# Kernel optimization log

Hardware: AMD Instinct MI355X
Metric: run time of the kernel (lower is better)

## Reference

```python
import jax, jax.numpy as jnp
import numpy as np

TWO_PI = 6.283185307179586


def setup_inputs() -> dict:
    key = jax.random.key(0)
    k1, k2, k3, k4, k5, k6 = jax.random.split(key, 6)
    B, T, D = 2, 8192, 1024
    x = jax.random.normal(k1, (B, T, D), dtype=jnp.float32)
    # nn.Linear weights are [out, in]; init with small scale like torch default
    s = 1.0 / np.sqrt(D)
    Wk = jax.random.uniform(k2, (D, D), jnp.float32, -s, s)
    Wv = jax.random.uniform(k3, (D, D), jnp.float32, -s, s)
    Wo = jax.random.uniform(k4, (D, D), jnp.float32, -s, s)
    # random phasor frequencies in [0, 2*pi)
    freqs = jax.random.uniform(k5, (D,), jnp.float32, 0.0, TWO_PI)
    return {"x": x, "Wk": Wk, "Wv": Wv, "Wo": Wo, "freqs": freqs}


def reference(x, Wk, Wv, Wo, freqs):
    B, T, C = x.shape
    # k projection is computed in the original forward but never used downstream
    k_real = x @ Wk.T  # [B,T,D] (dead value, kept for fidelity)
    v_real = x @ Wv.T  # [B,T,D]
    v = v_real.astype(jnp.complex64)
    # rotors: per-position unit phasors exp(i * t * freqs), shape [T, D]
    t = jnp.arange(T, dtype=jnp.float32)
    rotors = jnp.exp(1j * (t[:, None] * freqs[None, :])).astype(jnp.complex64)
    # bind each value with its rotor and accumulate causally (O(N) memory trace)
    memory_trace = jnp.cumsum(v * rotors[None, :, :], axis=1)  # [B,T,D] complex64
    # retrieve by unbinding with the conjugate rotor; take the real component
    retrieved = jnp.real(memory_trace * jnp.conj(rotors)[None, :, :])  # [B,T,D]
    return retrieved @ Wo.T
```

## Files before the change

### kernel.cpp

```cpp
#include <hip/hip_runtime.h>
#include <hip/hip_bf16.h>


#define B_  2
#define T_  8192
#define D_  1024
#define BT_ 16384
#define CS_ 32
#define NCHUNK_ 256

typedef __attribute__((ext_vector_type(4))) float f32x4;
typedef __attribute__((ext_vector_type(8))) short bf16x8;

static __device__ inline unsigned short f2bf(float f) {
    union { float f; unsigned int u; } a;
    a.f = f;
    unsigned int u = a.u;
    return (unsigned short)((u + 0x7FFFu + ((u >> 16) & 1u)) >> 16);
}
static __device__ inline float bf2f(unsigned short h) {
    union { unsigned int u; float f; } a;
    a.u = ((unsigned int)h) << 16;
    return a.f;
}

__global__ __launch_bounds__(256) void cast_all(const float* __restrict__ x,
                                                const float* __restrict__ Wv,
                                                const float* __restrict__ Wo,
                                                unsigned short* __restrict__ xb,
                                                unsigned short* __restrict__ wvb,
                                                unsigned short* __restrict__ wob) {
    const int nx = BT_ * D_ / 4;
    const int nw = D_ * D_ / 4;
    int i = blockIdx.x * 256 + threadIdx.x;
    const float4* src;
    unsigned short* dst;
    int j;
    if (i < nx)            { src = (const float4*)x;  dst = xb;  j = i; }
    else if (i < nx + nw)  { src = (const float4*)Wv; dst = wvb; j = i - nx; }
    else                   { src = (const float4*)Wo; dst = wob; j = i - nx - nw; }
    float4 v = src[j];
    ushort4 o;
    o.x = f2bf(v.x); o.y = f2bf(v.y); o.z = f2bf(v.z); o.w = f2bf(v.w);
    ((ushort4*)dst)[j] = o;
}

template <bool BF16OUT>
__global__ __launch_bounds__(256) void gemm_bt(const short* __restrict__ A,
                                               const short* __restrict__ Bm,
                                               void* __restrict__ Cout,
                                               int M, int N, int K) {
    __shared__ short lds[16384];
    const int lane = threadIdx.x & 63;
    const int wave = threadIdx.x >> 6;
    const int wr = wave >> 1, wc = wave & 1;

    const int nb = N >> 7;
    const int id = blockIdx.x;
    const int xcd = id & 7;
    const int slot = id >> 3;
    const int bn = (slot % nb) * 128;
    const int bm = (xcd * ((M >> 7) >> 3) + slot / nb) * 128;

    const int sr = lane >> 3;
    const int cb = lane & 7;
    const short* ga[4];
    const short* gb[4];
#pragma unroll
    for (int cc = 0; cc < 4; ++cc) {
        const int chunk = wave * 4 + cc;
        const int row = chunk * 8 + sr;
        const int col = (cb ^ (row & 7)) * 8;
        ga[cc] = A + (size_t)(bm + row) * K + col;
        gb[cc] = Bm + (size_t)(bn + row) * K + col;
    }

    const int c4r = lane >> 4;
    int aoff[4][2], boff[4][2];
#pragma unroll
    for (int i = 0; i < 4; ++i) {
        const int m = wr * 64 + (lane & 15) + i * 16;
        const int n = wc * 64 + (lane & 15) + i * 16;
#pragma unroll
        for (int ks = 0; ks < 2; ++ks) {
            aoff[i][ks] = m * 64 + (((ks * 4 + c4r) ^ (m & 7)) * 8);
            boff[i][ks] = 8192 + n * 64 + (((ks * 4 + c4r) ^ (n & 7)) * 8);
        }
    }

    f32x4 acc[4][4] = {};

    for (int k0 = 0; k0 < K; k0 += 64) {
#pragma unroll
        for (int cc = 0; cc < 4; ++cc) {
            const int chunk = wave * 4 + cc;
            __builtin_amdgcn_global_load_lds(
                (const __attribute__((address_space(1))) void*)(ga[cc] + k0),
                (__attribute__((address_space(3))) void*)&lds[chunk * 512], 16, 0, 0);
            __builtin_amdgcn_global_load_lds(
                (const __attribute__((address_space(1))) void*)(gb[cc] + k0),
                (__attribute__((address_space(3))) void*)&lds[8192 + chunk * 512], 16, 0, 0);
        }
        __syncthreads();
#pragma unroll
        for (int ks = 0; ks < 2; ++ks) {
            bf16x8 a[4], b[4];
#pragma unroll
            for (int i = 0; i < 4; ++i) a[i] = *(const bf16x8*)&lds[aoff[i][ks]];
#pragma unroll
            for (int j = 0; j < 4; ++j) b[j] = *(const bf16x8*)&lds[boff[j][ks]];
#pragma unroll
            for (int i = 0; i < 4; ++i)
#pragma unroll
                for (int j = 0; j < 4; ++j)
                    acc[i][j] = __builtin_amdgcn_mfma_f32_16x16x32_bf16(a[i], b[j], acc[i][j], 0, 0, 0);
        }
        __syncthreads();
    }

    const int row0 = (lane >> 4) * 4;
#pragma unroll
    for (int i = 0; i < 4; ++i) {
#pragma unroll
        for (int j = 0; j < 4; ++j) {
            const int col = bn + wc * 64 + j * 16 + (lane & 15);
#pragma unroll
            for (int r = 0; r < 4; ++r) {
                const size_t row = bm + wr * 64 + i * 16 + row0 + r;
                if constexpr (BF16OUT)
                    ((unsigned short*)Cout)[row * N + col] = f2bf(acc[i][j][r]);
                else
                    ((float*)Cout)[row * N + col] = acc[i][j][r];
            }
        }
    }
}

__global__ __launch_bounds__(256) void scan_pass1(const unsigned short* __restrict__ v,
                                                  const float* __restrict__ freqs,
                                                  float* __restrict__ csum) {
    const int d0 = threadIdx.x * 4;
    const int chunk = blockIdx.x;
    const int b = blockIdx.y;

    float fr[4], s[4], c[4], sf[4], cf[4], ar[4] = {}, ai[4] = {};
    {
        float4 f4 = *(const float4*)(freqs + d0);
        fr[0] = f4.x; fr[1] = f4.y; fr[2] = f4.z; fr[3] = f4.w;
    }
    const float t0f = (float)(chunk * CS_);
#pragma unroll
    for (int k = 0; k < 4; ++k) {
        sincosf(t0f * fr[k], &s[k], &c[k]);
        sincosf(fr[k], &sf[k], &cf[k]);
    }
    const uint2* vp = (const uint2*)(v + ((size_t)b * T_ + chunk * CS_) * D_ + d0);
    for (int tb = 0; tb < CS_; tb += 8) {
        uint2 w[8];
#pragma unroll
        for (int u = 0; u < 8; ++u) w[u] = vp[(size_t)(tb + u) * (D_ / 4)];
#pragma unroll
        for (int u = 0; u < 8; ++u) {
            float wv[4];
            wv[0] = bf2f((unsigned short)w[u].x);
            wv[1] = bf2f((unsigned short)(w[u].x >> 16));
            wv[2] = bf2f((unsigned short)w[u].y);
            wv[3] = bf2f((unsigned short)(w[u].y >> 16));
#pragma unroll
            for (int k = 0; k < 4; ++k) {
                ar[k] = fmaf(wv[k], c[k], ar[k]);
                ai[k] = fmaf(wv[k], s[k], ai[k]);
                float nc = c[k] * cf[k] - s[k] * sf[k];
                float ns = s[k] * cf[k] + c[k] * sf[k];
                c[k] = nc; s[k] = ns;
            }
        }
    }
    float4* cp = (float4*)(csum + (((size_t)b * NCHUNK_ + chunk) * D_ + d0) * 2);
    float4 o0, o1;
    o0.x = ar[0]; o0.y = ai[0]; o0.z = ar[1]; o0.w = ai[1];
    o1.x = ar[2]; o1.y = ai[2]; o1.z = ar[3]; o1.w = ai[3];
    cp[0] = o0; cp[1] = o1;
}

__global__ __launch_bounds__(256) void scan_pass2(float* __restrict__ csum) {
    const int g = blockIdx.x * 256 + threadIdx.x;
    const int b = g / D_;
    const int d = g % D_;
    float2* cs = (float2*)csum;
    const size_t base = (size_t)b * NCHUNK_ * D_ + d;
    float pr = 0.f, pi = 0.f;
    for (int cc = 0; cc < NCHUNK_; cc += 32) {
        float2 buf[32];
#pragma unroll
        for (int k = 0; k < 32; ++k) buf[k] = cs[base + (size_t)(cc + k) * D_];
#pragma unroll
        for (int k = 0; k < 32; ++k) {
            float r = buf[k].x, im = buf[k].y;
            buf[k] = make_float2(pr, pi);
            pr += r; pi += im;
        }
#pragma unroll
        for (int k = 0; k < 32; ++k) cs[base + (size_t)(cc + k) * D_] = buf[k];
    }
}

__global__ __launch_bounds__(256) void scan_pass3(const unsigned short* __restrict__ v,
                                                  const float* __restrict__ freqs,
                                                  const float* __restrict__ csum,
                                                  unsigned short* __restrict__ ret) {
    const int d0 = threadIdx.x * 4;
    const int chunk = blockIdx.x;
    const int b = blockIdx.y;

    float fr[4], s[4], c[4], sf[4], cf[4], ar[4], ai[4];
    {
        float4 f4 = *(const float4*)(freqs + d0);
        fr[0] = f4.x; fr[1] = f4.y; fr[2] = f4.z; fr[3] = f4.w;
    }
    const float t0f = (float)(chunk * CS_);
#pragma unroll
    for (int k = 0; k < 4; ++k) {
        sincosf(t0f * fr[k], &s[k], &c[k]);
        sincosf(fr[k], &sf[k], &cf[k]);
    }
    {
        const float4* cp = (const float4*)(csum + (((size_t)b * NCHUNK_ + chunk) * D_ + d0) * 2);
        float4 o0 = cp[0], o1 = cp[1];
        ar[0] = o0.x; ai[0] = o0.y; ar[1] = o0.z; ai[1] = o0.w;
        ar[2] = o1.x; ai[2] = o1.y; ar[3] = o1.z; ai[3] = o1.w;
    }
    const uint2* vp = (const uint2*)(v + ((size_t)b * T_ + chunk * CS_) * D_ + d0);
    uint2* rp = (uint2*)(ret + ((size_t)b * T_ + chunk * CS_) * D_ + d0);
    for (int tb = 0; tb < CS_; tb += 8) {
        uint2 w[8];
#pragma unroll
        for (int u = 0; u < 8; ++u) w[u] = vp[(size_t)(tb + u) * (D_ / 4)];
#pragma unroll
        for (int u = 0; u < 8; ++u) {
            float wv[4], o[4];
            wv[0] = bf2f((unsigned short)w[u].x);
            wv[1] = bf2f((unsigned short)(w[u].x >> 16));
            wv[2] = bf2f((unsigned short)w[u].y);
            wv[3] = bf2f((unsigned short)(w[u].y >> 16));
#pragma unroll
            for (int k = 0; k < 4; ++k) {
                ar[k] = fmaf(wv[k], c[k], ar[k]);
                ai[k] = fmaf(wv[k], s[k], ai[k]);
                o[k] = ar[k] * c[k] + ai[k] * s[k];
                float nc = c[k] * cf[k] - s[k] * sf[k];
                float ns = s[k] * cf[k] + c[k] * sf[k];
                c[k] = nc; s[k] = ns;
            }
            uint2 o2;
            o2.x = (unsigned int)f2bf(o[0]) | ((unsigned int)f2bf(o[1]) << 16);
            o2.y = (unsigned int)f2bf(o[2]) | ((unsigned int)f2bf(o[3]) << 16);
            rp[(size_t)(tb + u) * (D_ / 4)] = o2;
        }
    }
}

extern "C" void kernel_launch(void* const* d_in, const int* in_sizes, int n_in,
                              void* d_out, int out_size, void* d_ws, size_t ws_size,
                              hipStream_t stream) {
    const float* x     = (const float*)d_in[0];
    const float* Wv    = (const float*)d_in[2];
    const float* Wo    = (const float*)d_in[3];
    const float* freqs = (const float*)d_in[4];
    float* out = (float*)d_out;

    char* ws = (char*)d_ws;
    unsigned short* x_bf  = (unsigned short*)ws;
    unsigned short* Wv_bf = (unsigned short*)(ws + 33554432);
    unsigned short* Wo_bf = (unsigned short*)(ws + 35651584);
    unsigned short* ret   = (unsigned short*)(ws + 37748736);
    float*          csum  = (float*)(ws + 71303168);
    unsigned short* v_bf = (unsigned short*)d_out;

    cast_all<<<(BT_ * D_ / 4 + 2 * D_ * D_ / 4) / 256, 256, 0, stream>>>(
        x, Wv, Wo, x_bf, Wv_bf, Wo_bf);

    gemm_bt<true><<<(BT_ / 128) * (D_ / 128), 256, 0, stream>>>(
        (const short*)x_bf, (const short*)Wv_bf, (void*)v_bf, BT_, D_, D_);

    dim3 sgrid(NCHUNK_, B_);
    scan_pass1<<<sgrid, 256, 0, stream>>>(v_bf, freqs, csum);
    scan_pass2<<<(B_ * D_) / 256, 256, 0, stream>>>(csum);
    scan_pass3<<<sgrid, 256, 0, stream>>>(v_bf, freqs, csum, ret);

    gemm_bt<false><<<(BT_ / 128) * (D_ / 128), 256, 0, stream>>>(
        (const short*)ret, (const short*)Wo_bf, (void*)out, BT_, D_, D_);
}
```

Baseline: 257.3 us.

## Fuse per-chunk phasor sums into the V-projection GEMM epilogue

The scan's first pass, which computes rotated partial sums per chunk, moves into the epilogue of the V-projection GEMM. Each wave reduces its 64-row tile in registers with rotor recurrences and cross-lane shuffles, then writes the chunk sum directly. This removes one full re-read of the bf16 V tensor and one kernel launch. The chunk size doubles to match the GEMM tile height, and pass 3 is regridded to split D across blocks so its parallelism is unchanged. In exchange, the GEMM epilogue gains sincos and recurrence work, and the longer chunks carry rotor recurrences further, which may cost some accuracy.

```diff
diff --git a/kernel.cpp b/kernel.cpp
--- a/kernel.cpp
+++ b/kernel.cpp
@@ -6,8 +6,8 @@
 #define T_  8192
 #define D_  1024
 #define BT_ 16384
-#define CS_ 32
-#define NCHUNK_ 256
+#define CS_ 64
+#define NCHUNK_ 128
 
 typedef __attribute__((ext_vector_type(4))) float f32x4;
 typedef __attribute__((ext_vector_type(8))) short bf16x8;
@@ -45,10 +45,12 @@
     ((ushort4*)dst)[j] = o;
 }
 
-template <bool BF16OUT>
+template <bool BF16OUT, bool FUSE_SUMS>
 __global__ __launch_bounds__(256) void gemm_bt(const short* __restrict__ A,
                                                const short* __restrict__ Bm,
                                                void* __restrict__ Cout,
+                                               const float* __restrict__ freqs,
+                                               float* __restrict__ csum,
                                                int M, int N, int K) {
     __shared__ short lds[16384];
     const int lane = threadIdx.x & 63;
@@ -118,7 +120,7 @@
         __syncthreads();
     }
 
-    const int row0 = (lane >> 4) * 4;
+    const int row0 = c4r * 4;
 #pragma unroll
     for (int i = 0; i < 4; ++i) {
 #pragma unroll
@@ -134,53 +136,47 @@
             }
         }
     }
-}
-
-__global__ __launch_bounds__(256) void scan_pass1(const unsigned short* __restrict__ v,
-                                                  const float* __restrict__ freqs,
-                                                  float* __restrict__ csum) {
-    const int d0 = threadIdx.x * 4;
-    const int chunk = blockIdx.x;
-    const int b = blockIdx.y;
-
-    float fr[4], s[4], c[4], sf[4], cf[4], ar[4] = {}, ai[4] = {};
-    {
-        float4 f4 = *(const float4*)(freqs + d0);
-        fr[0] = f4.x; fr[1] = f4.y; fr[2] = f4.z; fr[3] = f4.w;
-    }
-    const float t0f = (float)(chunk * CS_);
-#pragma unroll
-    for (int k = 0; k < 4; ++k) {
-        sincosf(t0f * fr[k], &s[k], &c[k]);
-        sincosf(fr[k], &sf[k], &cf[k]);
-    }
-    const uint2* vp = (const uint2*)(v + ((size_t)b * T_ + chunk * CS_) * D_ + d0);
-    for (int tb = 0; tb < CS_; tb += 8) {
-        uint2 w[8];
-#pragma unroll
-        for (int u = 0; u < 8; ++u) w[u] = vp[(size_t)(tb + u) * (D_ / 4)];
-#pragma unroll
-        for (int u = 0; u < 8; ++u) {
-            float wv[4];
-            wv[0] = bf2f((unsigned short)w[u].x);
-            wv[1] = bf2f((unsigned short)(w[u].x >> 16));
-            wv[2] = bf2f((unsigned short)w[u].y);
-            wv[3] = bf2f((unsigned short)(w[u].y >> 16));
-#pragma unroll
-            for (int k = 0; k < 4; ++k) {
-                ar[k] = fmaf(wv[k], c[k], ar[k]);
-                ai[k] = fmaf(wv[k], s[k], ai[k]);
-                float nc = c[k] * cf[k] - s[k] * sf[k];
-                float ns = s[k] * cf[k] + c[k] * sf[k];
-                c[k] = nc; s[k] = ns;
+
+    if constexpr (FUSE_SUMS) {
+        const int b = bm >> 13;
+        const int trow = bm & 8191;
+        const int chunk = (trow >> 6) + wr;
+        const int t0 = trow + wr * 64 + c4r * 4;
+#pragma unroll
+        for (int j = 0; j < 4; ++j) {
+            const int d = bn + wc * 64 + j * 16 + (lane & 15);
+            const float f = freqs[d];
+            float ss, cc2;
+            sincosf((float)t0 * f, &ss, &cc2);
+            float s1, c1;
+            sincosf(f, &s1, &c1);
+            float c2 = c1 * c1 - s1 * s1, s2 = 2.f * c1 * s1;
+            float c4 = c2 * c2 - s2 * s2, s4 = 2.f * c2 * s2;
+            float c8 = c4 * c4 - s4 * s4, s8 = 2.f * c4 * s4;
+            float c12 = c8 * c4 - s8 * s4, s12 = s8 * c4 + c8 * s4;
+            float c13 = c12 * c1 - s12 * s1, s13 = s12 * c1 + c12 * s1;
+            float ar = 0.f, ai = 0.f;
+            float cr = cc2, sr2 = ss;
+#pragma unroll
+            for (int i = 0; i < 4; ++i) {
+#pragma unroll
+                for (int r = 0; r < 4; ++r) {
+                    const float w = acc[i][j][r];
+                    ar = fmaf(w, cr, ar); ai = fmaf(w, sr2, ai);
+                    const float ec = (r < 3) ? c1 : c13;
+                    const float es = (r < 3) ? s1 : s13;
+                    const float nc = cr * ec - sr2 * es;
+                    const float ns = sr2 * ec + cr * es;
+                    cr = nc; sr2 = ns;
+                }
             }
-        }
-    }
-    float4* cp = (float4*)(csum + (((size_t)b * NCHUNK_ + chunk) * D_ + d0) * 2);
-    float4 o0, o1;
-    o0.x = ar[0]; o0.y = ai[0]; o0.z = ar[1]; o0.w = ai[1];
-    o1.x = ar[2]; o1.y = ai[2]; o1.z = ar[3]; o1.w = ai[3];
-    cp[0] = o0; cp[1] = o1;
+            ar += __shfl_xor(ar, 16); ai += __shfl_xor(ai, 16);
+            ar += __shfl_xor(ar, 32); ai += __shfl_xor(ai, 32);
+            if (c4r == 0)
+                *(float2*)(csum + (((size_t)b * NCHUNK_ + chunk) * D_ + d) * 2) =
+                    make_float2(ar, ai);
+        }
+    }
 }
 
 __global__ __launch_bounds__(256) void scan_pass2(float* __restrict__ csum) {
@@ -209,42 +205,38 @@
                                                   const float* __restrict__ freqs,
                                                   const float* __restrict__ csum,
                                                   unsigned short* __restrict__ ret) {
-    const int d0 = threadIdx.x * 4;
     const int chunk = blockIdx.x;
-    const int b = blockIdx.y;
-
-    float fr[4], s[4], c[4], sf[4], cf[4], ar[4], ai[4];
+    const int d0 = blockIdx.y * 512 + threadIdx.x * 2;
+    const int b = blockIdx.z;
+
+    float fr[2], s[2], c[2], sf[2], cf[2], ar[2], ai[2];
     {
-        float4 f4 = *(const float4*)(freqs + d0);
-        fr[0] = f4.x; fr[1] = f4.y; fr[2] = f4.z; fr[3] = f4.w;
+        float2 f2 = *(const float2*)(freqs + d0);
+        fr[0] = f2.x; fr[1] = f2.y;
     }
     const float t0f = (float)(chunk * CS_);
 #pragma unroll
-    for (int k = 0; k < 4; ++k) {
+    for (int k = 0; k < 2; ++k) {
         sincosf(t0f * fr[k], &s[k], &c[k]);
         sincosf(fr[k], &sf[k], &cf[k]);
     }
     {
-        const float4* cp = (const float4*)(csum + (((size_t)b * NCHUNK_ + chunk) * D_ + d0) * 2);
-        float4 o0 = cp[0], o1 = cp[1];
-        ar[0] = o0.x; ai[0] = o0.y; ar[1] = o0.z; ai[1] = o0.w;
-        ar[2] = o1.x; ai[2] = o1.y; ar[3] = o1.z; ai[3] = o1.w;
-    }
-    const uint2* vp = (const uint2*)(v + ((size_t)b * T_ + chunk * CS_) * D_ + d0);
-    uint2* rp = (uint2*)(ret + ((size_t)b * T_ + chunk * CS_) * D_ + d0);
+        const float4 o = *(const float4*)(csum + (((size_t)b * NCHUNK_ + chunk) * D_ + d0) * 2);
+        ar[0] = o.x; ai[0] = o.y; ar[1] = o.z; ai[1] = o.w;
+    }
+    const unsigned int* vp = (const unsigned int*)(v + ((size_t)b * T_ + chunk * CS_) * D_ + d0);
+    unsigned int* rp = (unsigned int*)(ret + ((size_t)b * T_ + chunk * CS_) * D_ + d0);
     for (int tb = 0; tb < CS_; tb += 8) {
-        uint2 w[8];
-#pragma unroll
-        for (int u = 0; u < 8; ++u) w[u] = vp[(size_t)(tb + u) * (D_ / 4)];
+        unsigned int w[8];
+#pragma unroll
+        for (int u = 0; u < 8; ++u) w[u] = vp[(size_t)(tb + u) * (D_ / 2)];
 #pragma unroll
         for (int u = 0; u < 8; ++u) {
-            float wv[4], o[4];
-            wv[0] = bf2f((unsigned short)w[u].x);
-            wv[1] = bf2f((unsigned short)(w[u].x >> 16));
-            wv[2] = bf2f((unsigned short)w[u].y);
-            wv[3] = bf2f((unsigned short)(w[u].y >> 16));
-#pragma unroll
-            for (int k = 0; k < 4; ++k) {
+            float wv[2], o[2];
+            wv[0] = bf2f((unsigned short)w[u]);
+            wv[1] = bf2f((unsigned short)(w[u] >> 16));
+#pragma unroll
+            for (int k = 0; k < 2; ++k) {
                 ar[k] = fmaf(wv[k], c[k], ar[k]);
                 ai[k] = fmaf(wv[k], s[k], ai[k]);
                 o[k] = ar[k] * c[k] + ai[k] * s[k];
@@ -252,10 +244,8 @@
                 float ns = s[k] * cf[k] + c[k] * sf[k];
                 c[k] = nc; s[k] = ns;
             }
-            uint2 o2;
-            o2.x = (unsigned int)f2bf(o[0]) | ((unsigned int)f2bf(o[1]) << 16);
-            o2.y = (unsigned int)f2bf(o[2]) | ((unsigned int)f2bf(o[3]) << 16);
-            rp[(size_t)(tb + u) * (D_ / 4)] = o2;
+            rp[(size_t)(tb + u) * (D_ / 2)] =
+                (unsigned int)f2bf(o[0]) | ((unsigned int)f2bf(o[1]) << 16);
         }
     }
 }
@@ -280,14 +270,13 @@
     cast_all<<<(BT_ * D_ / 4 + 2 * D_ * D_ / 4) / 256, 256, 0, stream>>>(
         x, Wv, Wo, x_bf, Wv_bf, Wo_bf);
 
-    gemm_bt<true><<<(BT_ / 128) * (D_ / 128), 256, 0, stream>>>(
-        (const short*)x_bf, (const short*)Wv_bf, (void*)v_bf, BT_, D_, D_);
-
-    dim3 sgrid(NCHUNK_, B_);
-    scan_pass1<<<sgrid, 256, 0, stream>>>(v_bf, freqs, csum);
+    gemm_bt<true, true><<<(BT_ / 128) * (D_ / 128), 256, 0, stream>>>(
+        (const short*)x_bf, (const short*)Wv_bf, (void*)v_bf, freqs, csum, BT_, D_, D_);
+
     scan_pass2<<<(B_ * D_) / 256, 256, 0, stream>>>(csum);
-    scan_pass3<<<sgrid, 256, 0, stream>>>(v_bf, freqs, csum, ret);
-
-    gemm_bt<false><<<(BT_ / 128) * (D_ / 128), 256, 0, stream>>>(
-        (const short*)ret, (const short*)Wo_bf, (void*)out, BT_, D_, D_);
-}
+    dim3 p3grid(NCHUNK_, D_ / 512, B_);
+    scan_pass3<<<p3grid, 256, 0, stream>>>(v_bf, freqs, csum, ret);
+
+    gemm_bt<false, false><<<(BT_ / 128) * (D_ / 128), 256, 0, stream>>>(
+        (const short*)ret, (const short*)Wo_bf, (void*)out, nullptr, nullptr, BT_, D_, D_);
+}
```

After: 240.3 us. 6.6% less time.
